# Optimization experiments

Hardware: AMD Instinct MI355X
Metric: run time of the kernel (lower is better)

Reference implementation:

```python
import jax, jax.numpy as jnp
import numpy as np


def setup_inputs() -> dict:
    key = jax.random.key(0)
    ks = jax.random.split(key, 8)
    H, O, B, T = 1024, 512, 512, 256
    s_ih = 1.0 / np.sqrt(H)
    return {
        "h0": jax.random.normal(ks[0], (1, B, H), jnp.float32),
        "c0": jax.random.normal(ks[1], (1, B, H), jnp.float32),
        "W_ih": jax.random.normal(ks[2], (4 * H, O), jnp.float32) * s_ih,
        "W_hh": jax.random.normal(ks[3], (4 * H, H), jnp.float32) * s_ih,
        "b_ih": jax.random.normal(ks[4], (4 * H,), jnp.float32) * s_ih,
        "b_hh": jax.random.normal(ks[5], (4 * H,), jnp.float32) * s_ih,
        "W_out": jax.random.normal(ks[6], (O, H), jnp.float32) * s_ih,
        "b_out": jax.random.normal(ks[7], (O,), jnp.float32) * s_ih,
        "out_len": T,
    }


def reference(h0, c0, W_ih, W_hh, b_ih, b_hh, W_out, b_out, out_len):
    B = h0.shape[1]
    O = W_out.shape[0]
    h = h0.reshape(B, -1)  # [B, H]
    c = c0.reshape(B, -1)  # [B, H]
    x = jnp.zeros((B, O), dtype=h.dtype)  # initial lstm_in of zeros

    def step(carry, _):
        h, c, x = carry
        # PyTorch LSTMCell: gates ordered (i, f, g, o)
        gates = x @ W_ih.T + b_ih + h @ W_hh.T + b_hh  # [B, 4H]
        i, f, g, o = jnp.split(gates, 4, axis=-1)
        c_new = jax.nn.sigmoid(f) * c + jax.nn.sigmoid(i) * jnp.tanh(g)
        h_new = jax.nn.sigmoid(o) * jnp.tanh(c_new)
        y = jax.nn.softmax(h_new @ W_out.T + b_out, axis=-1)  # [B, O]
        return (h_new, c_new, y), y

    _, ys = jax.lax.scan(step, (h, c, x), None, length=out_len)
    # original writes output[i-1] for i = out_len..1, i.e. time-reversed storage
    return ys[::-1]  # [out_len, B, O]
```

## Files before the change

### kernel.cpp

```cpp
#include <hip/hip_runtime.h>
#include <math.h>

#define BB 512
#define HH 1024
#define OO 512
#define KC 1536
#define G4H 4096
#define TT 256

typedef _Float16 half8 __attribute__((ext_vector_type(8)));
typedef float f32x4 __attribute__((ext_vector_type(4)));

__device__ __forceinline__ void dma16(const void* g, void* l) {
    __builtin_amdgcn_global_load_lds(
        (const __attribute__((address_space(1))) void*)g,
        (__attribute__((address_space(3))) void*)l, 16, 0, 0);
}

__global__ __launch_bounds__(256) void conv_wcat(
    const float* __restrict__ W_ih, const float* __restrict__ W_hh,
    _Float16* __restrict__ Wcat)
{
    int k = blockIdx.x * 256 + threadIdx.x;
    int p = blockIdx.y;
    int g = (p >> 5) & 3, jt = p >> 7, jr = p & 31;
    int n = g * HH + jt * 32 + jr;
    float v = (k < OO) ? W_ih[(size_t)n * OO + k] : W_hh[(size_t)n * HH + (k - OO)];
    Wcat[(size_t)p * KC + k] = (_Float16)v;
}

__global__ __launch_bounds__(256) void conv_wout(
    const float* __restrict__ W_out, _Float16* __restrict__ Wout16)
{
    int k = blockIdx.x * 256 + threadIdx.x;
    int o = blockIdx.y;
    Wout16[(size_t)o * HH + k] = (_Float16)W_out[(size_t)o * HH + k];
}

__global__ __launch_bounds__(256) void prep_misc(
    const float* __restrict__ b_ih, const float* __restrict__ b_hh,
    const float* __restrict__ h0, const float* __restrict__ c0,
    float* __restrict__ bias_p, _Float16* __restrict__ hb0, float* __restrict__ cst)
{
    int idx0 = blockIdx.x * blockDim.x + threadIdx.x;
    int stride = gridDim.x * blockDim.x;
    for (int p = idx0; p < G4H; p += stride) {
        int g = (p >> 5) & 3, jt = p >> 7, jr = p & 31;
        int n = g * HH + jt * 32 + jr;
        bias_p[p] = b_ih[n] + b_hh[n];
    }
    for (int i = idx0; i < BB * HH; i += stride) {
        hb0[i] = (_Float16)h0[i];
        cst[i] = c0[i];
    }
}

__global__ __launch_bounds__(256) void gates_sf2(
    const float* __restrict__ ebuf,
    const float* __restrict__ Spart,
    const _Float16* __restrict__ h_in,
    _Float16* __restrict__ h_out,
    float* __restrict__ cst,
    const _Float16* __restrict__ Wcat,
    const float* __restrict__ bias_p,
    float* __restrict__ out_slice,
    int first)
{
    const int pt = blockIdx.x;
    const int p0 = pt * 128, b0 = blockIdx.y * 64;
    const int tid = threadIdx.x;
    const int l = tid & 63, w = tid >> 6;
    const int wm = w & 1, wn = w >> 1;
    const int l15 = l & 15, l4 = l >> 4;

    __shared__ __align__(16) char smem[49408];
    _Float16* Af = (_Float16*)smem;
    _Float16* Bf = (_Float16*)(smem + 16384);
    float* sm_inv = (float*)(smem + 49152);

    if (!first) {
        if (tid < 64) {
            const float* sp = &Spart[(size_t)(b0 + tid) * 16];
            float s = 0.f;
            #pragma unroll
            for (int u = 0; u < 16; ++u) s += sp[u];
            sm_inv[tid] = 1.f / s;
        }
        __syncthreads();
        int bl = pt * 2 + (tid >> 7);
        int col = (tid & 127) * 4;
        float inv = sm_inv[bl];
        float4 e4 = *(const float4*)&ebuf[(size_t)(b0 + bl) * OO + col];
        float4 y4 = {e4.x * inv, e4.y * inv, e4.z * inv, e4.w * inv};
        *(float4*)&out_slice[(size_t)(b0 + bl) * OO + col] = y4;
    }
    __syncthreads();

    f32x4 acc[2][4];
    #pragma unroll
    for (int fm = 0; fm < 2; ++fm)
        #pragma unroll
        for (int fn = 0; fn < 4; ++fn)
            acc[fm][fn] = (f32x4){0.f, 0.f, 0.f, 0.f};

    half8 ra[4], rb[8];

    auto load_regs = [&](int k0) {
        if (k0 < OO) {
            #pragma unroll
            for (int j = 0; j < 4; ++j) {
                int row = (w * 4 + j) * 4 + l4;
                int c = l15 ^ (row & 7);
                const float* lp = &ebuf[(size_t)(b0 + row) * OO + k0 + c * 8];
                float lv[8];
                *(float4*)&lv[0] = *(const float4*)lp;
                *(float4*)&lv[4] = *(const float4*)(lp + 4);
                float inv = sm_inv[row];
                #pragma unroll
                for (int e = 0; e < 8; ++e)
                    ra[j][e] = (_Float16)(lv[e] * inv);
            }
        } else {
            #pragma unroll
            for (int j = 0; j < 4; ++j) {
                int row = (w * 4 + j) * 4 + l4;
                int c = l15 ^ (row & 7);
                ra[j] = *(const half8*)&h_in[(size_t)(b0 + row) * HH + (k0 - OO) + c * 8];
            }
        }
        #pragma unroll
        for (int j = 0; j < 8; ++j) {
            int row = (w * 8 + j) * 4 + l4;
            int c = l15 ^ (row & 7);
            rb[j] = *(const half8*)&Wcat[(size_t)(p0 + row) * KC + k0 + c * 8];
        }
    };
    auto store_lds = [&]() {
        #pragma unroll
        for (int j = 0; j < 4; ++j)
            *(half8*)&Af[(size_t)(w * 4 + j) * 512 + l * 8] = ra[j];
        #pragma unroll
        for (int j = 0; j < 8; ++j)
            *(half8*)&Bf[(size_t)(w * 8 + j) * 512 + l * 8] = rb[j];
    };

    const int it0 = first ? 4 : 0;
    load_regs(it0 * 128);
    #pragma unroll 1
    for (int it = it0; it < KC / 128; ++it) {
        __syncthreads();
        store_lds();
        __syncthreads();
        if (it + 1 < KC / 128) load_regs((it + 1) * 128);

        #pragma unroll
        for (int ks = 0; ks < 4; ++ks) {
            int cc = (ks * 4 + l4) ^ (l15 & 7);
            half8 af[2], bfr[4];
            #pragma unroll
            for (int fm = 0; fm < 2; ++fm) {
                int R = wm * 32 + fm * 16 + l15;
                af[fm] = *(const half8*)&Af[R * 128 + cc * 8];
            }
            #pragma unroll
            for (int fn = 0; fn < 4; ++fn) {
                int S = wn * 64 + fn * 16 + l15;
                bfr[fn] = *(const half8*)&Bf[S * 128 + cc * 8];
            }
            #pragma unroll
            for (int fm = 0; fm < 2; ++fm)
                #pragma unroll
                for (int fn = 0; fn < 4; ++fn)
                    acc[fm][fn] = __builtin_amdgcn_mfma_f32_16x16x32_f16(
                        af[fm], bfr[fn], acc[fm][fn], 0, 0, 0);
        }
    }
    __syncthreads();

    float* exch = (float*)smem;
    #pragma unroll
    for (int fm = 0; fm < 2; ++fm)
        #pragma unroll
        for (int fn = 0; fn < 4; ++fn)
            #pragma unroll
            for (int r = 0; r < 4; ++r) {
                int row = wm * 32 + fm * 16 + l4 * 4 + r;
                int col = wn * 64 + fn * 16 + l15;
                exch[row * 133 + col] = acc[fm][fn][r];
            }
    __syncthreads();

    int bl = tid >> 2;
    int b = b0 + bl;
    int jbase = (tid & 3) * 8;
    float cv[8], hv[8], cold[8];
    *(float4*)&cold[0] = *(const float4*)&cst[(size_t)b * HH + pt * 32 + jbase];
    *(float4*)&cold[4] = *(const float4*)&cst[(size_t)b * HH + pt * 32 + jbase + 4];
    #pragma unroll
    for (int u = 0; u < 8; ++u) {
        int jr = jbase + u;
        float gi = exch[bl * 133 +      jr] + bias_p[p0 +      jr];
        float gf = exch[bl * 133 + 32 + jr] + bias_p[p0 + 32 + jr];
        float gg = exch[bl * 133 + 64 + jr] + bias_p[p0 + 64 + jr];
        float go = exch[bl * 133 + 96 + jr] + bias_p[p0 + 96 + jr];
        float iv = 1.f / (1.f + expf(-gi));
        float fv = 1.f / (1.f + expf(-gf));
        float gv = tanhf(gg);
        float ov = 1.f / (1.f + expf(-go));
        float cnew = fv * cold[u] + iv * gv;
        cv[u] = cnew;
        hv[u] = ov * tanhf(cnew);
    }
    *(float4*)&cst[(size_t)b * HH + pt * 32 + jbase]     = *(const float4*)&cv[0];
    *(float4*)&cst[(size_t)b * HH + pt * 32 + jbase + 4] = *(const float4*)&cv[4];
    half8 hh;
    #pragma unroll
    for (int u = 0; u < 8; ++u) hh[u] = (_Float16)hv[u];
    *(half8*)&h_out[(size_t)b * HH + pt * 32 + jbase] = hh;
}

__global__ __launch_bounds__(128) void logits_exp(
    const _Float16* __restrict__ hb,
    const _Float16* __restrict__ Wout16,
    const float* __restrict__ b_out,
    float* __restrict__ ebuf,
    float* __restrict__ Spart)
{
    const int ot = blockIdx.x;
    const int o0 = ot * 32, b0 = blockIdx.y * 32;
    const int tid = threadIdx.x;
    const int l = tid & 63, w = tid >> 6;
    const int l15 = l & 15, l4 = l >> 4, lo3 = l & 7;

    __shared__ __align__(16) _Float16 Ah[32 * 128];
    __shared__ __align__(16) _Float16 Bo[32 * 128];

    f32x4 acc[2];
    acc[0] = (f32x4){0.f, 0.f, 0.f, 0.f};
    acc[1] = (f32x4){0.f, 0.f, 0.f, 0.f};

    for (int k0 = 0; k0 < HH; k0 += 128) {
        #pragma unroll
        for (int j = 0; j < 4; ++j) {
            int row = (w * 4 + j) * 4 + l4;
            int c = l15 ^ (row & 7);
            dma16(&hb[(size_t)(b0 + row) * HH + k0 + c * 8],
                  &Ah[(size_t)(w * 4 + j) * 512]);
        }
        #pragma unroll
        for (int j = 0; j < 4; ++j) {
            int row = (w * 4 + j) * 4 + l4;
            int c = l15 ^ (row & 7);
            dma16(&Wout16[(size_t)(o0 + row) * HH + k0 + c * 8],
                  &Bo[(size_t)(w * 4 + j) * 512]);
        }
        __syncthreads();
        #pragma unroll
        for (int ks = 0; ks < 4; ++ks) {
            int cc = (ks * 4 + l4) ^ lo3;
            int R = w * 16 + l15;
            half8 a = *(const half8*)&Ah[R * 128 + cc * 8];
            #pragma unroll
            for (int fn = 0; fn < 2; ++fn) {
                int S = fn * 16 + l15;
                half8 bq = *(const half8*)&Bo[S * 128 + cc * 8];
                acc[fn] = __builtin_amdgcn_mfma_f32_16x16x32_f16(a, bq, acc[fn], 0, 0, 0);
            }
        }
        __syncthreads();
    }
    float ps[4] = {0.f, 0.f, 0.f, 0.f};
    #pragma unroll
    for (int fn = 0; fn < 2; ++fn)
        #pragma unroll
        for (int r = 0; r < 4; ++r) {
            int row = b0 + w * 16 + l4 * 4 + r;
            int col = o0 + fn * 16 + l15;
            float e = expf(acc[fn][r] + b_out[col]);
            ebuf[(size_t)row * OO + col] = e;
            ps[r] += e;
        }
    #pragma unroll
    for (int r = 0; r < 4; ++r) {
        #pragma unroll
        for (int off = 1; off < 16; off <<= 1)
            ps[r] += __shfl_xor(ps[r], off, 64);
    }
    if (l15 == 0) {
        #pragma unroll
        for (int r = 0; r < 4; ++r) {
            int row = b0 + w * 16 + l4 * 4 + r;
            Spart[(size_t)row * 16 + ot] = ps[r];
        }
    }
}

__global__ __launch_bounds__(256) void softmax_out(
    const float* __restrict__ ebuf, const float* __restrict__ Spart,
    float* __restrict__ out_slice)
{
    const int w = threadIdx.x >> 6, l = threadIdx.x & 63;
    const int b = blockIdx.x * 4 + w;
    const float* sp = &Spart[(size_t)b * 16];
    float s = 0.f;
    #pragma unroll
    for (int u = 0; u < 16; ++u) s += sp[u];
    float inv = 1.f / s;
    float v[8], y[8];
    *(float4*)&v[0] = *(const float4*)&ebuf[(size_t)b * OO + l * 8];
    *(float4*)&v[4] = *(const float4*)&ebuf[(size_t)b * OO + l * 8 + 4];
    #pragma unroll
    for (int u = 0; u < 8; ++u) y[u] = v[u] * inv;
    *(float4*)&out_slice[(size_t)b * OO + l * 8]     = *(const float4*)&y[0];
    *(float4*)&out_slice[(size_t)b * OO + l * 8 + 4] = *(const float4*)&y[4];
}

extern "C" void kernel_launch(void* const* d_in, const int* in_sizes, int n_in,
                              void* d_out, int out_size, void* d_ws, size_t ws_size,
                              hipStream_t stream)
{
    const float* h0    = (const float*)d_in[0];
    const float* c0    = (const float*)d_in[1];
    const float* W_ih  = (const float*)d_in[2];
    const float* W_hh  = (const float*)d_in[3];
    const float* b_ih  = (const float*)d_in[4];
    const float* b_hh  = (const float*)d_in[5];
    const float* W_out = (const float*)d_in[6];
    const float* b_out = (const float*)d_in[7];
    float* out = (float*)d_out;

    char* wsb = (char*)d_ws;
    _Float16* Wcat   = (_Float16*)wsb;                 wsb += (size_t)G4H * KC * 2;
    _Float16* Wout16 = (_Float16*)wsb;                 wsb += (size_t)OO * HH * 2;
    float*    bias_p = (float*)wsb;                    wsb += (size_t)G4H * 4;
    _Float16* hb0    = (_Float16*)wsb;                 wsb += (size_t)BB * HH * 2;
    _Float16* hb1    = (_Float16*)wsb;                 wsb += (size_t)BB * HH * 2;
    float*    cst    = (float*)wsb;                    wsb += (size_t)BB * HH * 4;
    float*    ebuf   = (float*)wsb;                    wsb += (size_t)BB * OO * 4;
    float*    Spart  = (float*)wsb;                    wsb += (size_t)BB * 16 * 4;

    conv_wcat<<<dim3(KC / 256, G4H), 256, 0, stream>>>(W_ih, W_hh, Wcat);
    conv_wout<<<dim3(HH / 256, OO), 256, 0, stream>>>(W_out, Wout16);
    prep_misc<<<512, 256, 0, stream>>>(b_ih, b_hh, h0, c0, bias_p, hb0, cst);

    for (int t = 0; t < TT; ++t) {
        _Float16* hin  = (t & 1) ? hb1 : hb0;
        _Float16* hout = (t & 1) ? hb0 : hb1;
        float* oslice = (t == 0) ? out : out + (size_t)(TT - t) * BB * OO;
        gates_sf2<<<dim3(32, 8), 256, 0, stream>>>(
            ebuf, Spart, hin, hout, cst, Wcat, bias_p, oslice, (t == 0) ? 1 : 0);
        logits_exp<<<dim3(16, 16), 128, 0, stream>>>(hout, Wout16, b_out, ebuf, Spart);
    }
    softmax_out<<<128, 256, 0, stream>>>(ebuf, Spart, out);
}
```

Baseline: 7.473 ms.

## Load MFMA operands directly from global memory, drop LDS staging, double waves

The LSTM gate GEMM and the output-logit GEMM now feed MFMA fragments straight from global memory instead of staging tiles through LDS with barriers. Block sizes double so each wave computes a smaller output tile, and softmax partial sums are split into 32 slices per row. The aim is to remove LDS round-trips and __syncthreads stalls in these latency-bound small GEMMs. The cost is strided, less coalesced global loads and duplicated operand fetches across waves, which now rely on L2 for reuse.

```diff
diff --git a/kernel.cpp b/kernel.cpp
--- a/kernel.cpp
+++ b/kernel.cpp
@@ -9,13 +9,8 @@
 #define TT 256
 
 typedef _Float16 half8 __attribute__((ext_vector_type(8)));
+typedef _Float16 half4 __attribute__((ext_vector_type(4)));
 typedef float f32x4 __attribute__((ext_vector_type(4)));
-
-__device__ __forceinline__ void dma16(const void* g, void* l) {
-    __builtin_amdgcn_global_load_lds(
-        (const __attribute__((address_space(1))) void*)g,
-        (__attribute__((address_space(3))) void*)l, 16, 0, 0);
-}
 
 __global__ __launch_bounds__(256) void conv_wcat(
     const float* __restrict__ W_ih, const float* __restrict__ W_hh,
@@ -55,7 +50,7 @@
     }
 }
 
-__global__ __launch_bounds__(256) void gates_sf2(
+__global__ __launch_bounds__(512) void gates_sf2(
     const float* __restrict__ ebuf,
     const float* __restrict__ Spart,
     const _Float16* __restrict__ h_in,
@@ -73,131 +68,120 @@
     const int wm = w & 1, wn = w >> 1;
     const int l15 = l & 15, l4 = l >> 4;
 
-    __shared__ __align__(16) char smem[49408];
-    _Float16* Af = (_Float16*)smem;
-    _Float16* Bf = (_Float16*)(smem + 16384);
-    float* sm_inv = (float*)(smem + 49152);
+    __shared__ __align__(16) char smem[34560];
+    float* exch   = (float*)smem;
+    float* sm_inv = (float*)(smem + 34048);
 
     if (!first) {
         if (tid < 64) {
-            const float* sp = &Spart[(size_t)(b0 + tid) * 16];
+            const float* sp = &Spart[(size_t)(b0 + tid) * 32];
             float s = 0.f;
             #pragma unroll
-            for (int u = 0; u < 16; ++u) s += sp[u];
+            for (int u = 0; u < 32; ++u) s += sp[u];
             sm_inv[tid] = 1.f / s;
         }
         __syncthreads();
-        int bl = pt * 2 + (tid >> 7);
-        int col = (tid & 127) * 4;
-        float inv = sm_inv[bl];
-        float4 e4 = *(const float4*)&ebuf[(size_t)(b0 + bl) * OO + col];
-        float4 y4 = {e4.x * inv, e4.y * inv, e4.z * inv, e4.w * inv};
-        *(float4*)&out_slice[(size_t)(b0 + bl) * OO + col] = y4;
+        if (tid < 256) {
+            int bl = pt * 2 + (tid >> 7);
+            int col = (tid & 127) * 4;
+            float inv = sm_inv[bl];
+            float4 e4 = *(const float4*)&ebuf[(size_t)(b0 + bl) * OO + col];
+            float4 y4 = {e4.x * inv, e4.y * inv, e4.z * inv, e4.w * inv};
+            *(float4*)&out_slice[(size_t)(b0 + bl) * OO + col] = y4;
+        }
     }
     __syncthreads();
 
-    f32x4 acc[2][4];
+    f32x4 acc[2][2];
     #pragma unroll
     for (int fm = 0; fm < 2; ++fm)
         #pragma unroll
-        for (int fn = 0; fn < 4; ++fn)
+        for (int fn = 0; fn < 2; ++fn)
             acc[fm][fn] = (f32x4){0.f, 0.f, 0.f, 0.f};
 
-    half8 ra[4], rb[8];
-
-    auto load_regs = [&](int k0) {
-        if (k0 < OO) {
+    const int rA0 = wm * 32 + l15, rA1 = wm * 32 + 16 + l15;
+    const float*    pE0 = &ebuf[(size_t)(b0 + rA0) * OO + l4 * 8];
+    const float*    pE1 = &ebuf[(size_t)(b0 + rA1) * OO + l4 * 8];
+    const _Float16* pH0 = &h_in[(size_t)(b0 + rA0) * HH + l4 * 8];
+    const _Float16* pH1 = &h_in[(size_t)(b0 + rA1) * HH + l4 * 8];
+    const _Float16* pB0 = &Wcat[(size_t)(p0 + wn * 32 +      l15) * KC + l4 * 8];
+    const _Float16* pB1 = &Wcat[(size_t)(p0 + wn * 32 + 16 + l15) * KC + l4 * 8];
+    const float invA0 = sm_inv[rA0];
+    const float invA1 = sm_inv[rA1];
+
+    if (!first) {
+        const float* e0 = pE0;
+        const float* e1 = pE1;
+        const _Float16* wb0 = pB0;
+        const _Float16* wb1 = pB1;
+        #pragma unroll 1
+        for (int it = 0; it < 4; ++it) {
             #pragma unroll
-            for (int j = 0; j < 4; ++j) {
-                int row = (w * 4 + j) * 4 + l4;
-                int c = l15 ^ (row & 7);
-                const float* lp = &ebuf[(size_t)(b0 + row) * OO + k0 + c * 8];
-                float lv[8];
-                *(float4*)&lv[0] = *(const float4*)lp;
-                *(float4*)&lv[4] = *(const float4*)(lp + 4);
-                float inv = sm_inv[row];
+            for (int ks = 0; ks < 4; ++ks) {
+                float lv0[8], lv1[8];
+                *(float4*)&lv0[0] = *(const float4*)(e0 + ks * 32);
+                *(float4*)&lv0[4] = *(const float4*)(e0 + ks * 32 + 4);
+                *(float4*)&lv1[0] = *(const float4*)(e1 + ks * 32);
+                *(float4*)&lv1[4] = *(const float4*)(e1 + ks * 32 + 4);
+                half8 af0, af1;
                 #pragma unroll
-                for (int e = 0; e < 8; ++e)
-                    ra[j][e] = (_Float16)(lv[e] * inv);
+                for (int e = 0; e < 8; ++e) {
+                    af0[e] = (_Float16)(lv0[e] * invA0);
+                    af1[e] = (_Float16)(lv1[e] * invA1);
+                }
+                half8 bq0 = *(const half8*)(wb0 + ks * 32);
+                half8 bq1 = *(const half8*)(wb1 + ks * 32);
+                acc[0][0] = __builtin_amdgcn_mfma_f32_16x16x32_f16(af0, bq0, acc[0][0], 0, 0, 0);
+                acc[0][1] = __builtin_amdgcn_mfma_f32_16x16x32_f16(af0, bq1, acc[0][1], 0, 0, 0);
+                acc[1][0] = __builtin_amdgcn_mfma_f32_16x16x32_f16(af1, bq0, acc[1][0], 0, 0, 0);
+                acc[1][1] = __builtin_amdgcn_mfma_f32_16x16x32_f16(af1, bq1, acc[1][1], 0, 0, 0);
             }
-        } else {
+            e0 += 128; e1 += 128; wb0 += 128; wb1 += 128;
+        }
+    }
+
+    {
+        const _Float16* a0 = pH0;
+        const _Float16* a1 = pH1;
+        const _Float16* wb0 = pB0 + OO;
+        const _Float16* wb1 = pB1 + OO;
+        #pragma unroll 1
+        for (int it = 0; it < 8; ++it) {
             #pragma unroll
-            for (int j = 0; j < 4; ++j) {
-                int row = (w * 4 + j) * 4 + l4;
-                int c = l15 ^ (row & 7);
-                ra[j] = *(const half8*)&h_in[(size_t)(b0 + row) * HH + (k0 - OO) + c * 8];
+            for (int ks = 0; ks < 4; ++ks) {
+                half8 af0 = *(const half8*)(a0 + ks * 32);
+                half8 af1 = *(const half8*)(a1 + ks * 32);
+                half8 bq0 = *(const half8*)(wb0 + ks * 32);
+                half8 bq1 = *(const half8*)(wb1 + ks * 32);
+                acc[0][0] = __builtin_amdgcn_mfma_f32_16x16x32_f16(af0, bq0, acc[0][0], 0, 0, 0);
+                acc[0][1] = __builtin_amdgcn_mfma_f32_16x16x32_f16(af0, bq1, acc[0][1], 0, 0, 0);
+                acc[1][0] = __builtin_amdgcn_mfma_f32_16x16x32_f16(af1, bq0, acc[1][0], 0, 0, 0);
+                acc[1][1] = __builtin_amdgcn_mfma_f32_16x16x32_f16(af1, bq1, acc[1][1], 0, 0, 0);
             }
-        }
-        #pragma unroll
-        for (int j = 0; j < 8; ++j) {
-            int row = (w * 8 + j) * 4 + l4;
-            int c = l15 ^ (row & 7);
-            rb[j] = *(const half8*)&Wcat[(size_t)(p0 + row) * KC + k0 + c * 8];
-        }
-    };
-    auto store_lds = [&]() {
-        #pragma unroll
-        for (int j = 0; j < 4; ++j)
-            *(half8*)&Af[(size_t)(w * 4 + j) * 512 + l * 8] = ra[j];
-        #pragma unroll
-        for (int j = 0; j < 8; ++j)
-            *(half8*)&Bf[(size_t)(w * 8 + j) * 512 + l * 8] = rb[j];
-    };
-
-    const int it0 = first ? 4 : 0;
-    load_regs(it0 * 128);
-    #pragma unroll 1
-    for (int it = it0; it < KC / 128; ++it) {
-        __syncthreads();
-        store_lds();
-        __syncthreads();
-        if (it + 1 < KC / 128) load_regs((it + 1) * 128);
-
-        #pragma unroll
-        for (int ks = 0; ks < 4; ++ks) {
-            int cc = (ks * 4 + l4) ^ (l15 & 7);
-            half8 af[2], bfr[4];
-            #pragma unroll
-            for (int fm = 0; fm < 2; ++fm) {
-                int R = wm * 32 + fm * 16 + l15;
-                af[fm] = *(const half8*)&Af[R * 128 + cc * 8];
-            }
-            #pragma unroll
-            for (int fn = 0; fn < 4; ++fn) {
-                int S = wn * 64 + fn * 16 + l15;
-                bfr[fn] = *(const half8*)&Bf[S * 128 + cc * 8];
-            }
-            #pragma unroll
-            for (int fm = 0; fm < 2; ++fm)
-                #pragma unroll
-                for (int fn = 0; fn < 4; ++fn)
-                    acc[fm][fn] = __builtin_amdgcn_mfma_f32_16x16x32_f16(
-                        af[fm], bfr[fn], acc[fm][fn], 0, 0, 0);
+            a0 += 128; a1 += 128; wb0 += 128; wb1 += 128;
         }
     }
     __syncthreads();
 
-    float* exch = (float*)smem;
     #pragma unroll
     for (int fm = 0; fm < 2; ++fm)
         #pragma unroll
-        for (int fn = 0; fn < 4; ++fn)
+        for (int fn = 0; fn < 2; ++fn)
             #pragma unroll
             for (int r = 0; r < 4; ++r) {
                 int row = wm * 32 + fm * 16 + l4 * 4 + r;
-                int col = wn * 64 + fn * 16 + l15;
+                int col = wn * 32 + fn * 16 + l15;
                 exch[row * 133 + col] = acc[fm][fn][r];
             }
     __syncthreads();
 
-    int bl = tid >> 2;
+    int bl = tid >> 3;
     int b = b0 + bl;
-    int jbase = (tid & 3) * 8;
-    float cv[8], hv[8], cold[8];
+    int jbase = (tid & 7) * 4;
+    float cv[4], hv[4], cold[4];
     *(float4*)&cold[0] = *(const float4*)&cst[(size_t)b * HH + pt * 32 + jbase];
-    *(float4*)&cold[4] = *(const float4*)&cst[(size_t)b * HH + pt * 32 + jbase + 4];
-    #pragma unroll
-    for (int u = 0; u < 8; ++u) {
+    #pragma unroll
+    for (int u = 0; u < 4; ++u) {
         int jr = jbase + u;
         float gi = exch[bl * 133 +      jr] + bias_p[p0 +      jr];
         float gf = exch[bl * 133 + 32 + jr] + bias_p[p0 + 32 + jr];
@@ -211,15 +195,14 @@
         cv[u] = cnew;
         hv[u] = ov * tanhf(cnew);
     }
-    *(float4*)&cst[(size_t)b * HH + pt * 32 + jbase]     = *(const float4*)&cv[0];
-    *(float4*)&cst[(size_t)b * HH + pt * 32 + jbase + 4] = *(const float4*)&cv[4];
-    half8 hh;
-    #pragma unroll
-    for (int u = 0; u < 8; ++u) hh[u] = (_Float16)hv[u];
-    *(half8*)&h_out[(size_t)b * HH + pt * 32 + jbase] = hh;
-}
-
-__global__ __launch_bounds__(128) void logits_exp(
+    *(float4*)&cst[(size_t)b * HH + pt * 32 + jbase] = *(const float4*)&cv[0];
+    half4 hh;
+    #pragma unroll
+    for (int u = 0; u < 4; ++u) hh[u] = (_Float16)hv[u];
+    *(half4*)&h_out[(size_t)b * HH + pt * 32 + jbase] = hh;
+}
+
+__global__ __launch_bounds__(256) void logits_exp(
     const _Float16* __restrict__ hb,
     const _Float16* __restrict__ Wout16,
     const float* __restrict__ b_out,
@@ -230,56 +213,34 @@
     const int o0 = ot * 32, b0 = blockIdx.y * 32;
     const int tid = threadIdx.x;
     const int l = tid & 63, w = tid >> 6;
-    const int l15 = l & 15, l4 = l >> 4, lo3 = l & 7;
-
-    __shared__ __align__(16) _Float16 Ah[32 * 128];
-    __shared__ __align__(16) _Float16 Bo[32 * 128];
-
-    f32x4 acc[2];
-    acc[0] = (f32x4){0.f, 0.f, 0.f, 0.f};
-    acc[1] = (f32x4){0.f, 0.f, 0.f, 0.f};
-
-    for (int k0 = 0; k0 < HH; k0 += 128) {
-        #pragma unroll
-        for (int j = 0; j < 4; ++j) {
-            int row = (w * 4 + j) * 4 + l4;
-            int c = l15 ^ (row & 7);
-            dma16(&hb[(size_t)(b0 + row) * HH + k0 + c * 8],
-                  &Ah[(size_t)(w * 4 + j) * 512]);
-        }
-        #pragma unroll
-        for (int j = 0; j < 4; ++j) {
-            int row = (w * 4 + j) * 4 + l4;
-            int c = l15 ^ (row & 7);
-            dma16(&Wout16[(size_t)(o0 + row) * HH + k0 + c * 8],
-                  &Bo[(size_t)(w * 4 + j) * 512]);
-        }
-        __syncthreads();
+    const int wm = w & 1, wn = w >> 1;
+    const int l15 = l & 15, l4 = l >> 4;
+
+    f32x4 acc = (f32x4){0.f, 0.f, 0.f, 0.f};
+
+    const _Float16* pA = &hb[(size_t)(b0 + wm * 16 + l15) * HH + l4 * 8];
+    const _Float16* pB = &Wout16[(size_t)(o0 + wn * 16 + l15) * HH + l4 * 8];
+
+    #pragma unroll 1
+    for (int it = 0; it < 8; ++it) {
         #pragma unroll
         for (int ks = 0; ks < 4; ++ks) {
-            int cc = (ks * 4 + l4) ^ lo3;
-            int R = w * 16 + l15;
-            half8 a = *(const half8*)&Ah[R * 128 + cc * 8];
-            #pragma unroll
-            for (int fn = 0; fn < 2; ++fn) {
-                int S = fn * 16 + l15;
-                half8 bq = *(const half8*)&Bo[S * 128 + cc * 8];
-                acc[fn] = __builtin_amdgcn_mfma_f32_16x16x32_f16(a, bq, acc[fn], 0, 0, 0);
-            }
-        }
-        __syncthreads();
-    }
-    float ps[4] = {0.f, 0.f, 0.f, 0.f};
-    #pragma unroll
-    for (int fn = 0; fn < 2; ++fn)
-        #pragma unroll
-        for (int r = 0; r < 4; ++r) {
-            int row = b0 + w * 16 + l4 * 4 + r;
-            int col = o0 + fn * 16 + l15;
-            float e = expf(acc[fn][r] + b_out[col]);
-            ebuf[(size_t)row * OO + col] = e;
-            ps[r] += e;
-        }
+            half8 a  = *(const half8*)(pA + ks * 32);
+            half8 bq = *(const half8*)(pB + ks * 32);
+            acc = __builtin_amdgcn_mfma_f32_16x16x32_f16(a, bq, acc, 0, 0, 0);
+        }
+        pA += 128; pB += 128;
+    }
+
+    float ps[4];
+    #pragma unroll
+    for (int r = 0; r < 4; ++r) {
+        int row = b0 + wm * 16 + l4 * 4 + r;
+        int col = o0 + wn * 16 + l15;
+        float e = expf(acc[r] + b_out[col]);
+        ebuf[(size_t)row * OO + col] = e;
+        ps[r] = e;
+    }
     #pragma unroll
     for (int r = 0; r < 4; ++r) {
         #pragma unroll
@@ -289,8 +250,8 @@
     if (l15 == 0) {
         #pragma unroll
         for (int r = 0; r < 4; ++r) {
-            int row = b0 + w * 16 + l4 * 4 + r;
-            Spart[(size_t)row * 16 + ot] = ps[r];
+            int row = b0 + wm * 16 + l4 * 4 + r;
+            Spart[(size_t)row * 32 + ot * 2 + wn] = ps[r];
         }
     }
 }
@@ -301,10 +262,10 @@
 {
     const int w = threadIdx.x >> 6, l = threadIdx.x & 63;
     const int b = blockIdx.x * 4 + w;
-    const float* sp = &Spart[(size_t)b * 16];
+    const float* sp = &Spart[(size_t)b * 32];
     float s = 0.f;
     #pragma unroll
-    for (int u = 0; u < 16; ++u) s += sp[u];
+    for (int u = 0; u < 32; ++u) s += sp[u];
     float inv = 1.f / s;
     float v[8], y[8];
     *(float4*)&v[0] = *(const float4*)&ebuf[(size_t)b * OO + l * 8];
@@ -337,7 +298,7 @@
     _Float16* hb1    = (_Float16*)wsb;                 wsb += (size_t)BB * HH * 2;
     float*    cst    = (float*)wsb;                    wsb += (size_t)BB * HH * 4;
     float*    ebuf   = (float*)wsb;                    wsb += (size_t)BB * OO * 4;
-    float*    Spart  = (float*)wsb;                    wsb += (size_t)BB * 16 * 4;
+    float*    Spart  = (float*)wsb;                    wsb += (size_t)BB * 32 * 4;
 
     conv_wcat<<<dim3(KC / 256, G4H), 256, 0, stream>>>(W_ih, W_hh, Wcat);
     conv_wout<<<dim3(HH / 256, OO), 256, 0, stream>>>(W_out, Wout16);
@@ -347,9 +308,9 @@
         _Float16* hin  = (t & 1) ? hb1 : hb0;
         _Float16* hout = (t & 1) ? hb0 : hb1;
         float* oslice = (t == 0) ? out : out + (size_t)(TT - t) * BB * OO;
-        gates_sf2<<<dim3(32, 8), 256, 0, stream>>>(
+        gates_sf2<<<dim3(32, 8), 512, 0, stream>>>(
             ebuf, Spart, hin, hout, cst, Wcat, bias_p, oslice, (t == 0) ? 1 : 0);
-        logits_exp<<<dim3(16, 16), 128, 0, stream>>>(hout, Wout16, b_out, ebuf, Spart);
+        logits_exp<<<dim3(16, 16), 256, 0, stream>>>(hout, Wout16, b_out, ebuf, Spart);
     }
     softmax_out<<<128, 256, 0, stream>>>(ebuf, Spart, out);
 }
```

Measured after the change: 16.91 ms. 126% more time.
